# Performance work log

Measured on AMD Instinct MI355X. Metric: run time of the kernel, lower is better.

## Reference

```python
import jax, jax.numpy as jnp
import numpy as np

NUM_CAPSULE = 16
DIM_CAPSULE = 16
NUM_ROUTINGS = 3
EPS = 1e-7  # K.epsilon()


def squash(v, axis=-1):
    # vectors * ||v||^2 / ((1+||v||^2) * ||v||)
    sn = jnp.sum(v * v, axis=axis, keepdims=True)
    return v * (sn / ((1.0 + sn) * jnp.sqrt(sn + EPS)))


def setup_inputs() -> dict:
    key = jax.random.key(0)
    k1, k2 = jax.random.split(key)
    B, I, Din = 64, 2048, 8
    inputs = jax.random.normal(k1, (B, I, Din), dtype=jnp.float32)
    # he_normal init: std = sqrt(2 / fan_in), fan_in = Din
    W = jax.random.normal(k2, (I, NUM_CAPSULE, Din, DIM_CAPSULE), dtype=jnp.float32) * np.float32(np.sqrt(2.0 / Din))
    return {"inputs": inputs, "W": W}


def reference(inputs, W):
    # inputs: [B, I, Din]; W: [I, K, Din, Dout]
    # u_hat[b,i,k,:] = inputs[b,i,:] @ W[i,k,:,:]  (replaces tile + per-batch matmul scan)
    u_hat = jnp.einsum('bid,ikde->bike', inputs, W)  # [B, I, K, Dout]
    B, I, Kc, _ = u_hat.shape
    b = jnp.zeros((B, I, Kc), dtype=u_hat.dtype)  # routing logits (bias)
    v = None
    for r in range(NUM_ROUTINGS):
        c = jax.nn.softmax(b, axis=2)                       # coupling over output capsules
        s = jnp.einsum('bik,bike->bke', c, u_hat)           # weighted sum over input capsules
        v = squash(s)                                       # [B, K, Dout]
        if r < NUM_ROUTINGS - 1:
            b = b + jnp.einsum('bike,bke->bik', u_hat, v)   # agreement update
    return v  # [B, num_capsule, dim_capsule]
```

## Files before the change

### kernel.cpp

```cpp
#include <hip/hip_runtime.h>
#include <hip/hip_cooperative_groups.h>
#include <cstddef>

namespace cg = cooperative_groups;

constexpr int Bn = 64;
constexpr int In = 2048;
constexpr int Dk = 8;
constexpr int Kc = 16;
constexpr int En = 16;
constexpr float EPS = 1e-7f;

constexpr int IB   = 8;
constexpr int P    = In / IB;
constexpr int BSET = 16;
constexpr int NBG  = Bn / BSET;
constexpr int BLOCKS = P * NBG;
constexpr int NXCD = 8;
constexpr int PPX  = P / NXCD;

template<int CTRL>
__device__ __forceinline__ float dpp_add(float v) {
    int r = __builtin_amdgcn_update_dpp(0, __float_as_int(v), CTRL, 0xF, 0xF, true);
    return v + __int_as_float(r);
}

template<bool UNIFORM>
__device__ __forceinline__ void iter_body(const float* __restrict__ smemx,
        const float* __restrict__ W, const float* __restrict__ vsg,
        float* __restrict__ partial, int p, int b0, int i0, int t)
{
    const int lane = t & 63;
    const int wv   = t >> 6;
    const int k    = lane >> 2;
    const int e4   = (lane & 3) << 2;
    const int bw   = b0 + (wv << 2);

    float4 vb[4];
    if (!UNIFORM) {
        #pragma unroll
        for (int b4 = 0; b4 < 4; ++b4)
            vb[b4] = *(const float4*)(vsg + ((bw + b4) << 8) + k * 16 + e4);
    }

    float4 acc[4];
    #pragma unroll
    for (int b4 = 0; b4 < 4; ++b4) acc[b4] = make_float4(0.f, 0.f, 0.f, 0.f);

    #pragma unroll 1
    for (int ii = 0; ii < IB; ++ii) {
        const int i = i0 + ii;
        const float* wp = W + (size_t)i * (Kc * Dk * En) + k * (Dk * En) + e4;
        float4 w[8];
        #pragma unroll
        for (int d = 0; d < 8; ++d) w[d] = *(const float4*)(wp + d * En);

        #pragma unroll
        for (int b4 = 0; b4 < 4; ++b4) {
            const int bl = (wv << 2) + b4;
            const float* xp = smemx + (((bl << 3) + ii) << 3);
            const float4 x0 = *(const float4*)xp;
            const float4 x1 = *(const float4*)(xp + 4);
            const float xs8[8] = {x0.x, x0.y, x0.z, x0.w, x1.x, x1.y, x1.z, x1.w};

            float4 uh = make_float4(0.f, 0.f, 0.f, 0.f);
            #pragma unroll
            for (int d = 0; d < 8; ++d) {
                uh.x = fmaf(xs8[d], w[d].x, uh.x);
                uh.y = fmaf(xs8[d], w[d].y, uh.y);
                uh.z = fmaf(xs8[d], w[d].z, uh.z);
                uh.w = fmaf(xs8[d], w[d].w, uh.w);
            }

            if (UNIFORM) {
                acc[b4].x += uh.x; acc[b4].y += uh.y;
                acc[b4].z += uh.z; acc[b4].w += uh.w;
            } else {
                float tt = uh.x * vb[b4].x + uh.y * vb[b4].y
                         + uh.z * vb[b4].z + uh.w * vb[b4].w;
                tt = dpp_add<0xB1>(tt);
                tt = dpp_add<0x4E>(tt);
                const float pe = __expf(tt);
                float den = dpp_add<0x124>(pe);
                den = dpp_add<0x128>(den);
                den += __shfl_xor(den, 16);
                den += __shfl_xor(den, 32);
                const float c = pe * __builtin_amdgcn_rcpf(den);
                acc[b4].x = fmaf(c, uh.x, acc[b4].x);
                acc[b4].y = fmaf(c, uh.y, acc[b4].y);
                acc[b4].z = fmaf(c, uh.z, acc[b4].z);
                acc[b4].w = fmaf(c, uh.w, acc[b4].w);
            }
        }
    }

    #pragma unroll
    for (int b4 = 0; b4 < 4; ++b4)
        *(float4*)(partial + ((size_t)(bw + b4) * P + p) * 256 + k * 16 + e4) = acc[b4];
}

__device__ __forceinline__ void reduce_phase(float* smem,
        const float* __restrict__ partial, float scale,
        const float* __restrict__ vprev, float* __restrict__ vout, int rb, int t)
{
    const int b  = rb >> 2;
    const int q  = rb & 3;
    const int t4 = t & 63;
    const int pg = t >> 6;
    const int el = (q << 6) + t4;
    const float* pp = partial + (size_t)b * (P * 256) + ((pg << 6) * 256) + el;

    float s0 = 0.f, s1 = 0.f, s2 = 0.f, s3 = 0.f;
    #pragma unroll 4
    for (int j = 0; j < 64; j += 4) {
        s0 += pp[(j + 0) * 256];
        s1 += pp[(j + 1) * 256];
        s2 += pp[(j + 2) * 256];
        s3 += pp[(j + 3) * 256];
    }
    float* red = smem + 1024;
    red[(pg << 6) + t4] = (s0 + s1) + (s2 + s3);
    __syncthreads();

    if (t < 64) {
        const float val = (red[t4] + red[64 + t4] + red[128 + t4] + red[192 + t4]) * scale;
        float sq = val * val;
        sq += __shfl_xor(sq, 1);
        sq += __shfl_xor(sq, 2);
        sq += __shfl_xor(sq, 4);
        sq += __shfl_xor(sq, 8);
        const float f = sq / ((1.0f + sq) * sqrtf(sq + EPS));
        float v = val * f;
        if (vprev) v += vprev[(b << 8) + el];
        vout[(b << 8) + el] = v;
    }
    __syncthreads();
}

__device__ __forceinline__ void tile_map(int bid, int& p, int& b0, int& i0) {
    const int xcd = bid & 7;
    const int j   = bid >> 3;
    p  = xcd * PPX + (j & (PPX - 1));
    b0 = (j >> 5) * BSET;
    i0 = p * IB;
}

__device__ __forceinline__ void stage_x(float* smem, const float* __restrict__ x,
                                        int b0, int i0, int t) {
    const int bl = t >> 4;
    const int r  = t & 15;
    ((float4*)smem)[t] = *(const float4*)(x + ((size_t)(b0 + bl) * In + i0) * Dk + (r << 2));
}

__global__ __launch_bounds__(256)
void caps_fused(const float* __restrict__ x, const float* __restrict__ W,
                float* __restrict__ partial, float* __restrict__ v0,
                float* __restrict__ vs, float* __restrict__ out)
{
    cg::grid_group grid = cg::this_grid();
    __shared__ __align__(16) float smem[2048];

    const int t = threadIdx.x, bid = blockIdx.x;
    int p, b0, i0;
    tile_map(bid, p, b0, i0);

    stage_x(smem, x, b0, i0, t);
    __syncthreads();

    iter_body<true>(smem, W, nullptr, partial, p, b0, i0, t);
    grid.sync();
    if (bid < 256) reduce_phase(smem, partial, 1.0f / 16.0f, nullptr, v0, bid, t);
    grid.sync();

    iter_body<false>(smem, W, v0, partial, p, b0, i0, t);
    grid.sync();
    if (bid < 256) reduce_phase(smem, partial, 1.0f, v0, vs, bid, t);
    grid.sync();

    iter_body<false>(smem, W, vs, partial, p, b0, i0, t);
    grid.sync();
    if (bid < 256) reduce_phase(smem, partial, 1.0f, nullptr, out, bid, t);
}

template<bool UNIFORM>
__global__ __launch_bounds__(256)
void caps_iter_g(const float* __restrict__ x, const float* __restrict__ W,
                 const float* __restrict__ vsg, float* __restrict__ partial)
{
    __shared__ __align__(16) float smem[2048];
    const int t = threadIdx.x;
    int p, b0, i0;
    tile_map(blockIdx.x, p, b0, i0);
    stage_x(smem, x, b0, i0, t);
    __syncthreads();
    iter_body<UNIFORM>(smem, W, vsg, partial, p, b0, i0, t);
}

__global__ __launch_bounds__(256)
void caps_reduce_g(const float* __restrict__ partial, float scale,
                   const float* __restrict__ vprev, float* __restrict__ vout)
{
    __shared__ __align__(16) float smem[2048];
    reduce_phase(smem, partial, scale, vprev, vout, blockIdx.x, threadIdx.x);
}

extern "C" void kernel_launch(void* const* d_in, const int* in_sizes, int n_in,
                              void* d_out, int out_size, void* d_ws, size_t ws_size,
                              hipStream_t stream) {
    const float* x = (const float*)d_in[0];
    const float* W = (const float*)d_in[1];
    float* out = (float*)d_out;
    float* ws  = (float*)d_ws;

    float* v0      = ws;
    float* vs      = ws + 16384;
    float* partial = ws + 32768;

    int dev = 0;
    hipGetDevice(&dev);
    int numCU = 0;
    hipDeviceGetAttribute(&numCU, hipDeviceAttributeMultiprocessorCount, dev);
    int maxB = 0;
    hipError_t oe = hipOccupancyMaxActiveBlocksPerMultiprocessor(
        &maxB, (const void*)caps_fused, 256, 0);
    const bool coop = (oe == hipSuccess) && numCU > 0 &&
                      ((long)maxB * numCU >= BLOCKS);

    if (coop) {
        void* args[] = { (void*)&x, (void*)&W, (void*)&partial,
                         (void*)&v0, (void*)&vs, (void*)&out };
        hipLaunchCooperativeKernel((void*)caps_fused, dim3(BLOCKS), dim3(256),
                                   args, 0, stream);
    } else {
        caps_iter_g<true ><<<BLOCKS, 256, 0, stream>>>(x, W, nullptr, partial);
        caps_reduce_g<<<256, 256, 0, stream>>>(partial, 1.0f / 16.0f, nullptr, v0);
        caps_iter_g<false><<<BLOCKS, 256, 0, stream>>>(x, W, v0, partial);
        caps_reduce_g<<<256, 256, 0, stream>>>(partial, 1.0f, v0, vs);
        caps_iter_g<false><<<BLOCKS, 256, 0, stream>>>(x, W, vs, partial);
        caps_reduce_g<<<256, 256, 0, stream>>>(partial, 1.0f, nullptr, out);
    }
}
```

Measured before the change: 64.07 us.

## Double-buffer W loads in registers and read x directly instead of via LDS

Replaces the shared-memory staging of x with direct wave-uniform global loads (the wave index is made scalar via readfirstlane, so the x loads can become scalar loads). The i loop is fully unrolled with two register buffers of W so the next input capsule's weights are fetched while the current one is computed. LDS usage shrinks to a 256-float reduction buffer, removing a __syncthreads and staging per block. This raises register pressure and re-reads x from global/cache in each routing iteration.

Measured after the change: 85.96 us. 34.2% more time.

```diff
diff --git a/kernel.cpp b/kernel.cpp
--- a/kernel.cpp
+++ b/kernel.cpp
@@ -16,8 +16,7 @@
 constexpr int BSET = 16;
 constexpr int NBG  = Bn / BSET;
 constexpr int BLOCKS = P * NBG;
-constexpr int NXCD = 8;
-constexpr int PPX  = P / NXCD;
+constexpr int PPX  = P / 8;
 
 template<int CTRL>
 __device__ __forceinline__ float dpp_add(float v) {
@@ -25,13 +24,21 @@
     return v + __int_as_float(r);
 }
 
+__device__ __forceinline__ void load_w(float4 (&w)[8], const float* __restrict__ W,
+                                       int i, int k, int e4) {
+    const float* wp = W + (size_t)i * (Kc * Dk * En) + k * (Dk * En) + e4;
+    #pragma unroll
+    for (int d = 0; d < 8; ++d) w[d] = *(const float4*)(wp + d * En);
+}
+
 template<bool UNIFORM>
-__device__ __forceinline__ void iter_body(const float* __restrict__ smemx,
-        const float* __restrict__ W, const float* __restrict__ vsg,
-        float* __restrict__ partial, int p, int b0, int i0, int t)
+__device__ __forceinline__ void iter_body(
+        const float* __restrict__ x, const float* __restrict__ W,
+        const float* __restrict__ vsg, float* __restrict__ partial,
+        int p, int b0, int i0, int t)
 {
     const int lane = t & 63;
-    const int wv   = t >> 6;
+    const int wv   = __builtin_amdgcn_readfirstlane(t >> 6);
     const int k    = lane >> 2;
     const int e4   = (lane & 3) << 2;
     const int bw   = b0 + (wv << 2);
@@ -47,50 +54,56 @@
     #pragma unroll
     for (int b4 = 0; b4 < 4; ++b4) acc[b4] = make_float4(0.f, 0.f, 0.f, 0.f);
 
-    #pragma unroll 1
-    for (int ii = 0; ii < IB; ++ii) {
-        const int i = i0 + ii;
-        const float* wp = W + (size_t)i * (Kc * Dk * En) + k * (Dk * En) + e4;
-        float4 w[8];
+    float4 w0[8], w1[8];
+    load_w(w0, W, i0, k, e4);
+
+    #pragma unroll
+    for (int ii = 0; ii < IB; ii += 2) {
+        load_w(w1, W, i0 + ii + 1, k, e4);
+
         #pragma unroll
-        for (int d = 0; d < 8; ++d) w[d] = *(const float4*)(wp + d * En);
-
-        #pragma unroll
-        for (int b4 = 0; b4 < 4; ++b4) {
-            const int bl = (wv << 2) + b4;
-            const float* xp = smemx + (((bl << 3) + ii) << 3);
-            const float4 x0 = *(const float4*)xp;
-            const float4 x1 = *(const float4*)(xp + 4);
-            const float xs8[8] = {x0.x, x0.y, x0.z, x0.w, x1.x, x1.y, x1.z, x1.w};
-
-            float4 uh = make_float4(0.f, 0.f, 0.f, 0.f);
+        for (int half = 0; half < 2; ++half) {
+            const int i = i0 + ii + half;
+            const float4 (&w)[8] = half ? w1 : w0;
+
             #pragma unroll
-            for (int d = 0; d < 8; ++d) {
-                uh.x = fmaf(xs8[d], w[d].x, uh.x);
-                uh.y = fmaf(xs8[d], w[d].y, uh.y);
-                uh.z = fmaf(xs8[d], w[d].z, uh.z);
-                uh.w = fmaf(xs8[d], w[d].w, uh.w);
+            for (int b4 = 0; b4 < 4; ++b4) {
+                const float* xp = x + ((size_t)(bw + b4) * In + i) * Dk;
+                const float4 x0 = *(const float4*)xp;
+                const float4 x1 = *(const float4*)(xp + 4);
+                const float xs8[8] = {x0.x, x0.y, x0.z, x0.w,
+                                      x1.x, x1.y, x1.z, x1.w};
+
+                float4 uh = make_float4(0.f, 0.f, 0.f, 0.f);
+                #pragma unroll
+                for (int d = 0; d < 8; ++d) {
+                    uh.x = fmaf(xs8[d], w[d].x, uh.x);
+                    uh.y = fmaf(xs8[d], w[d].y, uh.y);
+                    uh.z = fmaf(xs8[d], w[d].z, uh.z);
+                    uh.w = fmaf(xs8[d], w[d].w, uh.w);
+                }
+
+                if (UNIFORM) {
+                    acc[b4].x += uh.x; acc[b4].y += uh.y;
+                    acc[b4].z += uh.z; acc[b4].w += uh.w;
+                } else {
+                    float tt = uh.x * vb[b4].x + uh.y * vb[b4].y
+                             + uh.z * vb[b4].z + uh.w * vb[b4].w;
+                    tt = dpp_add<0xB1>(tt);
+                    tt = dpp_add<0x4E>(tt);
+                    const float pe = __expf(tt);
+                    float den = dpp_add<0x124>(pe);
+                    den = dpp_add<0x128>(den);
+                    den += __shfl_xor(den, 16);
+                    den += __shfl_xor(den, 32);
+                    const float c = pe * __builtin_amdgcn_rcpf(den);
+                    acc[b4].x = fmaf(c, uh.x, acc[b4].x);
+                    acc[b4].y = fmaf(c, uh.y, acc[b4].y);
+                    acc[b4].z = fmaf(c, uh.z, acc[b4].z);
+                    acc[b4].w = fmaf(c, uh.w, acc[b4].w);
+                }
             }
-
-            if (UNIFORM) {
-                acc[b4].x += uh.x; acc[b4].y += uh.y;
-                acc[b4].z += uh.z; acc[b4].w += uh.w;
-            } else {
-                float tt = uh.x * vb[b4].x + uh.y * vb[b4].y
-                         + uh.z * vb[b4].z + uh.w * vb[b4].w;
-                tt = dpp_add<0xB1>(tt);
-                tt = dpp_add<0x4E>(tt);
-                const float pe = __expf(tt);
-                float den = dpp_add<0x124>(pe);
-                den = dpp_add<0x128>(den);
-                den += __shfl_xor(den, 16);
-                den += __shfl_xor(den, 32);
-                const float c = pe * __builtin_amdgcn_rcpf(den);
-                acc[b4].x = fmaf(c, uh.x, acc[b4].x);
-                acc[b4].y = fmaf(c, uh.y, acc[b4].y);
-                acc[b4].z = fmaf(c, uh.z, acc[b4].z);
-                acc[b4].w = fmaf(c, uh.w, acc[b4].w);
-            }
+            if (half == 0 && ii + 2 < IB) load_w(w0, W, i0 + ii + 2, k, e4);
         }
     }
 
@@ -99,7 +112,7 @@
         *(float4*)(partial + ((size_t)(bw + b4) * P + p) * 256 + k * 16 + e4) = acc[b4];
 }
 
-__device__ __forceinline__ void reduce_phase(float* smem,
+__device__ __forceinline__ void reduce_phase(float* red,
         const float* __restrict__ partial, float scale,
         const float* __restrict__ vprev, float* __restrict__ vout, int rb, int t)
 {
@@ -118,7 +131,6 @@
         s2 += pp[(j + 2) * 256];
         s3 += pp[(j + 3) * 256];
     }
-    float* red = smem + 1024;
     red[(pg << 6) + t4] = (s0 + s1) + (s2 + s3);
     __syncthreads();
 
@@ -145,41 +157,31 @@
     i0 = p * IB;
 }
 
-__device__ __forceinline__ void stage_x(float* smem, const float* __restrict__ x,
-                                        int b0, int i0, int t) {
-    const int bl = t >> 4;
-    const int r  = t & 15;
-    ((float4*)smem)[t] = *(const float4*)(x + ((size_t)(b0 + bl) * In + i0) * Dk + (r << 2));
-}
-
 __global__ __launch_bounds__(256)
 void caps_fused(const float* __restrict__ x, const float* __restrict__ W,
                 float* __restrict__ partial, float* __restrict__ v0,
                 float* __restrict__ vs, float* __restrict__ out)
 {
     cg::grid_group grid = cg::this_grid();
-    __shared__ __align__(16) float smem[2048];
+    __shared__ __align__(16) float red[256];
 
     const int t = threadIdx.x, bid = blockIdx.x;
     int p, b0, i0;
     tile_map(bid, p, b0, i0);
 
-    stage_x(smem, x, b0, i0, t);
-    __syncthreads();
-
-    iter_body<true>(smem, W, nullptr, partial, p, b0, i0, t);
-    grid.sync();
-    if (bid < 256) reduce_phase(smem, partial, 1.0f / 16.0f, nullptr, v0, bid, t);
-    grid.sync();
-
-    iter_body<false>(smem, W, v0, partial, p, b0, i0, t);
-    grid.sync();
-    if (bid < 256) reduce_phase(smem, partial, 1.0f, v0, vs, bid, t);
-    grid.sync();
-
-    iter_body<false>(smem, W, vs, partial, p, b0, i0, t);
-    grid.sync();
-    if (bid < 256) reduce_phase(smem, partial, 1.0f, nullptr, out, bid, t);
+    iter_body<true>(x, W, nullptr, partial, p, b0, i0, t);
+    grid.sync();
+    if (bid < 256) reduce_phase(red, partial, 1.0f / 16.0f, nullptr, v0, bid, t);
+    grid.sync();
+
+    iter_body<false>(x, W, v0, partial, p, b0, i0, t);
+    grid.sync();
+    if (bid < 256) reduce_phase(red, partial, 1.0f, v0, vs, bid, t);
+    grid.sync();
+
+    iter_body<false>(x, W, vs, partial, p, b0, i0, t);
+    grid.sync();
+    if (bid < 256) reduce_phase(red, partial, 1.0f, nullptr, out, bid, t);
 }
 
 template<bool UNIFORM>
@@ -187,21 +189,17 @@
 void caps_iter_g(const float* __restrict__ x, const float* __restrict__ W,
                  const float* __restrict__ vsg, float* __restrict__ partial)
 {
-    __shared__ __align__(16) float smem[2048];
-    const int t = threadIdx.x;
     int p, b0, i0;
     tile_map(blockIdx.x, p, b0, i0);
-    stage_x(smem, x, b0, i0, t);
-    __syncthreads();
-    iter_body<UNIFORM>(smem, W, vsg, partial, p, b0, i0, t);
+    iter_body<UNIFORM>(x, W, vsg, partial, p, b0, i0, threadIdx.x);
 }
 
 __global__ __launch_bounds__(256)
 void caps_reduce_g(const float* __restrict__ partial, float scale,
                    const float* __restrict__ vprev, float* __restrict__ vout)
 {
-    __shared__ __align__(16) float smem[2048];
-    reduce_phase(smem, partial, scale, vprev, vout, blockIdx.x, threadIdx.x);
+    __shared__ __align__(16) float red[256];
+    reduce_phase(red, partial, scale, vprev, vout, blockIdx.x, threadIdx.x);
 }
 
 extern "C" void kernel_launch(void* const* d_in, const int* in_sizes, int n_in,
```
